# Kernel optimization log

Measured on AMD Instinct MI355X. Metric: run time of the kernel, lower is better.

Reference implementation:

```python
import jax, jax.numpy as jnp
import numpy as np

B, T, E, H = 2, 2048, 1024, 16
HS = E // H  # head size 64


def setup_inputs() -> dict:
    key = jax.random.key(0)
    ks = jax.random.split(key, 6)
    s = 0.02
    return {
        "x": jax.random.normal(ks[0], (B, T, E), dtype=jnp.float32),
        "Wq": jax.random.normal(ks[1], (E, E), dtype=jnp.float32) * s,
        "Wk": jax.random.normal(ks[2], (E, E), dtype=jnp.float32) * s,
        "Wv": jax.random.normal(ks[3], (E, E), dtype=jnp.float32) * s,
        "Wp": jax.random.normal(ks[4], (E, E), dtype=jnp.float32) * s,
        "bp": jax.random.normal(ks[5], (E,), dtype=jnp.float32) * s,
    }


def reference(x, Wq, Wk, Wv, Wp, bp):
    b, t, e = x.shape
    # per-head projections (concatenated heads == single E->E matmul, reshaped)
    def heads(w):
        return jnp.einsum('bte,ef->btf', x, w).reshape(b, t, H, HS).transpose(0, 2, 1, 3)
    q, k, v = heads(Wq), heads(Wk), heads(Wv)  # [B,H,T,HS]
    # NOTE: original scales by full embed dim E, not head_size
    scores = jnp.einsum('bhqd,bhkd->bhqk', q, k) * (e ** -0.5)
    causal = jnp.tril(jnp.ones((t, t), dtype=bool))
    scores = jnp.where(causal, scores, -jnp.inf)
    probs = jax.nn.softmax(scores, axis=-1)
    # dropout is identity in eval mode
    out = jnp.einsum('bhqk,bhkd->bhqd', probs, v)  # [B,H,T,HS]
    out = out.transpose(0, 2, 1, 3).reshape(b, t, e)
    return jnp.einsum('bte,ef->btf', out, Wp) + bp
```

## Files before the change

kernel.cpp:

```cpp
#include <hip/hip_runtime.h>
#include <math.h>

typedef __bf16 bf16x8 __attribute__((ext_vector_type(8)));
typedef __bf16 bf16x4 __attribute__((ext_vector_type(4)));
typedef float f32x4 __attribute__((ext_vector_type(4)));

constexpr int Bb = 2, Tt = 2048, Ee = 1024, Hh = 16, Hs = 64;
constexpr int Mm = Bb * Tt;

__device__ inline unsigned short f2bf(float f) {
    union { float f; unsigned u; } c; c.f = f;
    unsigned u = c.u;
    u += 0x7FFFu + ((u >> 16) & 1u);
    return (unsigned short)(u >> 16);
}

#if __has_builtin(__builtin_amdgcn_exp2f)
#define EXP2(x) __builtin_amdgcn_exp2f(x)
#else
#define EXP2(x) exp2f(x)
#endif

__device__ inline void gl2lds16(const void* g, void* l) {
    __builtin_amdgcn_global_load_lds(
        (const __attribute__((address_space(1))) void*)g,
        (__attribute__((address_space(3))) void*)l, 16, 0, 0);
}

__device__ inline unsigned pk_bf16(float a, float b) {
    union { float f; unsigned u; } ca, cb;
    ca.f = a; cb.f = b;
    return __builtin_amdgcn_perm(ca.u + 0x8000u, cb.u + 0x8000u, 0x07060302u);
}

__global__ __launch_bounds__(256) void prep(const float* __restrict__ x,
                                            const float* __restrict__ Wq,
                                            const float* __restrict__ Wk,
                                            const float* __restrict__ Wv,
                                            const float* __restrict__ Wp,
                                            unsigned short* __restrict__ xb,
                                            unsigned short* __restrict__ wt3,
                                            unsigned short* __restrict__ wpt) {
    const int tid = threadIdx.x;
    if (blockIdx.z == 4) {
        int flat = (blockIdx.y * 16 + blockIdx.x) * 256 + tid;
#pragma unroll
        for (int i = 0; i < 16; i++) {
            int gid = flat + i * 65536;
            float4 v = ((const float4*)x)[gid];
            ushort4 o;
            o.x = f2bf(v.x); o.y = f2bf(v.y); o.z = f2bf(v.z); o.w = f2bf(v.w);
            ((ushort4*)xb)[gid] = o;
        }
        return;
    }
    __shared__ unsigned short t[64][68];
    const float* W = (blockIdx.z == 0) ? Wq : (blockIdx.z == 1) ? Wk
                    : (blockIdx.z == 2) ? Wv : Wp;
    unsigned short* dst = (blockIdx.z < 3) ? wt3 + (size_t)blockIdx.z * 1024 * 1024 : wpt;
    const int k0 = blockIdx.x * 64, n0 = blockIdx.y * 64;
#pragma unroll
    for (int j = 0; j < 4; j++) {
        int row = (tid >> 4) + j * 16;
        int c4 = (tid & 15) * 4;
        float4 v = *(const float4*)&W[(size_t)(k0 + row) * 1024 + n0 + c4];
        t[row][c4 + 0] = f2bf(v.x); t[row][c4 + 1] = f2bf(v.y);
        t[row][c4 + 2] = f2bf(v.z); t[row][c4 + 3] = f2bf(v.w);
    }
    __syncthreads();
#pragma unroll
    for (int j = 0; j < 16; j++) {
        int flat = j * 256 + tid;
        int orow = flat >> 6, ocol = flat & 63;
        dst[(size_t)(n0 + orow) * 1024 + k0 + ocol] = t[ocol][orow];
    }
}

__device__ inline void gemm_mainloop(const unsigned short* __restrict__ A,
                                     const unsigned short* __restrict__ Bt,
                                     unsigned short* As, unsigned short* Bs,
                                     int bm, int bn, int tid, f32x4 (&acc)[4][4]) {
    const int lane = tid & 63, w = tid >> 6;
    const int quad = lane >> 4, cl = lane & 15;
    const int wm = (w >> 1) * 64, wn = (w & 1) * 64;

    auto stage = [&](int k0) {
#pragma unroll
        for (int i = 0; i < 2; i++) {
            int L = tid + i * 256;
            int r = L >> 2;
            int kc = (L & 3) ^ (r & 3);
            gl2lds16(A + (size_t)(bm + r) * 1024 + k0 + kc * 8, &As[L * 8]);
        }
#pragma unroll
        for (int i = 0; i < 2; i++) {
            int L = tid + i * 256;
            int r = L >> 2;
            int kc = (L & 3) ^ (r & 3);
            gl2lds16(Bt + (size_t)(bn + r) * 1024 + k0 + kc * 8, &Bs[L * 8]);
        }
    };

    stage(0);
    __syncthreads();
    for (int k0 = 0;;) {
        bf16x8 af[4], bfr[4];
#pragma unroll
        for (int mt = 0; mt < 4; mt++) {
            int r = wm + mt * 16 + cl;
            af[mt] = *(const bf16x8*)&As[(r * 4 + (quad ^ (r & 3))) * 8];
            int rb = wn + mt * 16 + cl;
            bfr[mt] = *(const bf16x8*)&Bs[(rb * 4 + (quad ^ (rb & 3))) * 8];
        }
#pragma unroll
        for (int mt = 0; mt < 4; mt++)
#pragma unroll
            for (int nt = 0; nt < 4; nt++)
                acc[mt][nt] = __builtin_amdgcn_mfma_f32_16x16x32_bf16(
                    af[mt], bfr[nt], acc[mt][nt], 0, 0, 0);
        k0 += 32;
        if (k0 >= 1024) break;
        __syncthreads();
        stage(k0);
        __syncthreads();
    }
}

__global__ __launch_bounds__(256, 2) void gemm_qkv(const unsigned short* __restrict__ A,
                                                   const unsigned short* __restrict__ Bt,
                                                   unsigned short* __restrict__ qb,
                                                   unsigned short* __restrict__ kb,
                                                   unsigned short* __restrict__ vtb) {
    __shared__ unsigned short As[128 * 32];
    __shared__ unsigned short Bs[128 * 32];
    const int tid = threadIdx.x;
    const int bm = blockIdx.y * 128;
    const int bn = blockIdx.x * 128;
    f32x4 acc[4][4] = {};
    gemm_mainloop(A, Bt, As, Bs, bm, bn, tid, acc);

    const int lane = tid & 63, w = tid >> 6;
    const int quad = lane >> 4, cl = lane & 15;
    const int wm = (w >> 1) * 64, wn = (w & 1) * 64;
    const int region = bn >> 10;

    if (region < 2) {
        unsigned short* dst = region ? kb : qb;
        const float qs = region ? 1.0f : 0.045084220027780107f;
#pragma unroll
        for (int mt = 0; mt < 4; mt++)
#pragma unroll
            for (int nt = 0; nt < 4; nt++)
#pragma unroll
                for (int rg = 0; rg < 4; rg++) {
                    int m = bm + wm + mt * 16 + quad * 4 + rg;
                    int nn = (bn + wn + nt * 16 + cl) & 1023;
                    int b = m >> 11, t = m & 2047, h = nn >> 6, hs = nn & 63;
                    dst[((size_t)(b * 16 + h) * 2048 + t) * 64 + hs] =
                        f2bf(acc[mt][nt][rg] * qs);
                }
    } else {
#pragma unroll
        for (int mt = 0; mt < 4; mt++) {
            int m0 = bm + wm + mt * 16 + quad * 4;
            int b = m0 >> 11, t0 = m0 & 2047;
#pragma unroll
            for (int nt = 0; nt < 4; nt++) {
                int nn = (bn + wn + nt * 16 + cl) & 1023;
                int h = nn >> 6, hs = nn & 63;
                ushort4 pk;
                pk.x = f2bf(acc[mt][nt][0]); pk.y = f2bf(acc[mt][nt][1]);
                pk.z = f2bf(acc[mt][nt][2]); pk.w = f2bf(acc[mt][nt][3]);
                *(ushort4*)&vtb[((size_t)(b * 16 + h) * 64 + hs) * 2048 + t0] = pk;
            }
        }
    }
}

__global__ __launch_bounds__(256, 4) void gemm_out(const unsigned short* __restrict__ A,
                                                   const unsigned short* __restrict__ Bt,
                                                   const float* __restrict__ bias,
                                                   float* __restrict__ out) {
    __shared__ unsigned short As[64 * 32];
    __shared__ unsigned short Bs[128 * 32];
    const int tid = threadIdx.x;
    const int bm = blockIdx.y * 64;
    const int bn = blockIdx.x * 128;
    const int lane = tid & 63, w = tid >> 6;
    const int quad = lane >> 4, cl = lane & 15;
    const int wm = (w >> 1) * 32, wn = (w & 1) * 64;
    f32x4 acc[2][4] = {};

    auto stage = [&](int k0) {
        {
            int L = tid;
            int r = L >> 2;
            int kc = (L & 3) ^ (r & 3);
            gl2lds16(A + (size_t)(bm + r) * 1024 + k0 + kc * 8, &As[L * 8]);
        }
#pragma unroll
        for (int i = 0; i < 2; i++) {
            int L = tid + i * 256;
            int r = L >> 2;
            int kc = (L & 3) ^ (r & 3);
            gl2lds16(Bt + (size_t)(bn + r) * 1024 + k0 + kc * 8, &Bs[L * 8]);
        }
    };

    stage(0);
    __syncthreads();
    for (int k0 = 0;;) {
        bf16x8 af[2], bfr[4];
#pragma unroll
        for (int mt = 0; mt < 2; mt++) {
            int r = wm + mt * 16 + cl;
            af[mt] = *(const bf16x8*)&As[(r * 4 + (quad ^ (r & 3))) * 8];
        }
#pragma unroll
        for (int nt = 0; nt < 4; nt++) {
            int rb = wn + nt * 16 + cl;
            bfr[nt] = *(const bf16x8*)&Bs[(rb * 4 + (quad ^ (rb & 3))) * 8];
        }
#pragma unroll
        for (int mt = 0; mt < 2; mt++)
#pragma unroll
            for (int nt = 0; nt < 4; nt++)
                acc[mt][nt] = __builtin_amdgcn_mfma_f32_16x16x32_bf16(
                    af[mt], bfr[nt], acc[mt][nt], 0, 0, 0);
        k0 += 32;
        if (k0 >= 1024) break;
        __syncthreads();
        stage(k0);
        __syncthreads();
    }

#pragma unroll
    for (int mt = 0; mt < 2; mt++)
#pragma unroll
        for (int nt = 0; nt < 4; nt++)
#pragma unroll
            for (int rg = 0; rg < 4; rg++) {
                int m = bm + wm + mt * 16 + quad * 4 + rg;
                int n = bn + wn + nt * 16 + cl;
                out[(size_t)m * 1024 + n] = acc[mt][nt][rg] + bias[n];
            }
}

__global__ __launch_bounds__(256, 2) void attn_mfma(const unsigned short* __restrict__ qg,
                                                    const unsigned short* __restrict__ kg,
                                                    const unsigned short* __restrict__ vtg,
                                                    unsigned short* __restrict__ og) {
    __shared__ unsigned short lds[36864];
    float* Cmb = (float*)lds;
    float* Ll = (float*)(lds + 8704);

    const int tid = threadIdx.x;
    const int idx = blockIdx.x;
    const int bh = idx & 31;
    const int qt = 31 - (idx >> 5);
    const int lane = tid & 63, w = tid >> 6;
    const int quad = lane >> 4, cl = lane & 15;
    const int p = w >> 1;
    const int qhalf = w & 1;
    const int qbase = qt * 64;
    const unsigned short* qB = qg + (size_t)bh * 2048 * 64;
    const unsigned short* kB = kg + (size_t)bh * 2048 * 64;
    const unsigned short* vB = vtg + (size_t)bh * 64 * 2048;

    auto stageKV = [&](int kt) {
        unsigned short* Kd = lds + (kt & 3) * 4096;
        unsigned short* Vd = lds + 16384 + (kt & 3) * 4096;
#pragma unroll
        for (int i = 0; i < 2; i++) {
            int L = tid + i * 256;
            int r = L >> 3;
            int kc = (L & 7) ^ (r & 7);
            gl2lds16(kB + (size_t)(kt * 64 + r) * 64 + kc * 8, &Kd[L * 8]);
            gl2lds16(vB + (size_t)r * 2048 + kt * 64 + kc * 8, &Vd[L * 8]);
        }
    };

    bf16x8 qf[2][2];
#pragma unroll
    for (int nt2 = 0; nt2 < 2; nt2++)
#pragma unroll
        for (int kf = 0; kf < 2; kf++) {
            int row = qbase + qhalf * 32 + nt2 * 16 + cl;
            qf[nt2][kf] = *(const bf16x8*)&qB[(size_t)row * 64 + (kf * 4 + quad) * 8];
        }

    bf16x8 ones;
#pragma unroll
    for (int i = 0; i < 8; i++) ones[i] = (__bf16)1.0f;

    f32x4 oacc[2][4] = {};
    f32x4 lacc[2] = {};
    unsigned short* Pw = lds + 32768 + w * 1024;
    const int nit = (qt + 2) >> 1;

    stageKV(0);
    if (qt >= 1) stageKV(1);
    __syncthreads();

    for (int i = 0; i < nit; i++) {
        if (2 * i + 2 <= qt) stageKV(2 * i + 2);
        if (2 * i + 3 <= qt) stageKV(2 * i + 3);

        const int kt = 2 * i + p;
        if (kt <= qt) {
            const bool diag = (kt == qt);
            const unsigned short* Kl = lds + (kt & 3) * 4096;
            const unsigned short* Vl = lds + 16384 + (kt & 3) * 4096;
            f32x4 sac[4][2] = {};
#pragma unroll
            for (int kf = 0; kf < 2; kf++)
#pragma unroll
                for (int mt = 0; mt < 4; mt++) {
                    int r = mt * 16 + cl, cc = kf * 4 + quad;
                    bf16x8 kf8 = *(const bf16x8*)&Kl[(r * 8 + (cc ^ (r & 7))) * 8];
#pragma unroll
                    for (int nt2 = 0; nt2 < 2; nt2++)
                        sac[mt][nt2] = __builtin_amdgcn_mfma_f32_16x16x32_bf16(
                            kf8, qf[nt2][kf], sac[mt][nt2], 0, 0, 0);
                }
#pragma unroll
            for (int ks = 0; ks < 2; ks++) {
#pragma unroll
                for (int mtl = 0; mtl < 2; mtl++)
#pragma unroll
                    for (int nt2 = 0; nt2 < 2; nt2++) {
                        float pv[4];
#pragma unroll
                        for (int rg = 0; rg < 4; rg++) {
                            float e = EXP2(sac[ks * 2 + mtl][nt2][rg]);
                            if (diag && (ks * 32 + mtl * 16 + quad * 4 + rg >
                                         nt2 * 16 + cl + qhalf * 32))
                                e = 0.0f;
                            pv[rg] = e;
                        }
                        uint2 d;
                        d.x = pk_bf16(pv[1], pv[0]);
                        d.y = pk_bf16(pv[3], pv[2]);
                        int r2 = nt2 * 16 + cl;
                        int c = mtl * 2 + (quad >> 1);
                        int pc = c ^ ((r2 >> 1) & 3);
                        *(uint2*)&Pw[r2 * 32 + pc * 8 + (quad & 1) * 4] = d;
                    }
                bf16x8 pf[2];
#pragma unroll
                for (int mt2 = 0; mt2 < 2; mt2++) {
                    int r2 = mt2 * 16 + cl;
                    int pc = quad ^ ((r2 >> 1) & 3);
                    pf[mt2] = *(const bf16x8*)&Pw[r2 * 32 + pc * 8];
                }
#pragma unroll
                for (int mt2 = 0; mt2 < 2; mt2++)
                    lacc[mt2] = __builtin_amdgcn_mfma_f32_16x16x32_bf16(
                        pf[mt2], ones, lacc[mt2], 0, 0, 0);
#pragma unroll
                for (int nt = 0; nt < 4; nt++) {
                    int r = nt * 16 + cl, cc = ks * 4 + quad;
                    bf16x8 vf = *(const bf16x8*)&Vl[(r * 8 + (cc ^ (r & 7))) * 8];
#pragma unroll
                    for (int mt2 = 0; mt2 < 2; mt2++)
                        oacc[mt2][nt] = __builtin_amdgcn_mfma_f32_16x16x32_bf16(
                            pf[mt2], vf, oacc[mt2][nt], 0, 0, 0);
                }
            }
        }
        __syncthreads();
    }

    if (p == 1) {
#pragma unroll
        for (int mt2 = 0; mt2 < 2; mt2++)
#pragma unroll
            for (int rg = 0; rg < 4; rg++) {
                int row = qhalf * 32 + mt2 * 16 + quad * 4 + rg;
                if (cl == 0) Ll[row] = lacc[mt2][rg];
#pragma unroll
                for (int nt = 0; nt < 4; nt++)
                    Cmb[row * 68 + nt * 16 + cl] = oacc[mt2][nt][rg];
            }
    }
    __syncthreads();
    if (p == 0) {
        const int b = bh >> 4, h = bh & 15;
#pragma unroll
        for (int mt2 = 0; mt2 < 2; mt2++)
#pragma unroll
            for (int rg = 0; rg < 4; rg++) {
                int row = qhalf * 32 + mt2 * 16 + quad * 4 + rg;
                float inv = 1.0f / (lacc[mt2][rg] + Ll[row]);
                int t = qbase + row;
#pragma unroll
                for (int nt = 0; nt < 4; nt++) {
                    int hs = nt * 16 + cl;
                    float val = oacc[mt2][nt][rg] + Cmb[row * 68 + nt * 16 + cl];
                    og[((size_t)(b * 2048 + t)) * 1024 + h * 64 + hs] = f2bf(val * inv);
                }
            }
    }
}

extern "C" void kernel_launch(void* const* d_in, const int* in_sizes, int n_in,
                              void* d_out, int out_size, void* d_ws, size_t ws_size,
                              hipStream_t stream) {
    const float* x = (const float*)d_in[0];
    const float* Wq = (const float*)d_in[1];
    const float* Wk = (const float*)d_in[2];
    const float* Wv = (const float*)d_in[3];
    const float* Wp = (const float*)d_in[4];
    const float* bp = (const float*)d_in[5];
    float* out = (float*)d_out;

    unsigned short* xb = (unsigned short*)d_ws;
    unsigned short* wt3 = xb + (size_t)Mm * Ee;
    unsigned short* wpt = wt3 + (size_t)3 * Ee * Ee;
    unsigned short* qb = wpt + (size_t)Ee * Ee;
    unsigned short* kb = qb + (size_t)Mm * Ee;
    unsigned short* vtb = kb + (size_t)Mm * Ee;
    unsigned short* ab = vtb + (size_t)Mm * Ee;

    prep<<<dim3(16, 16, 5), dim3(256), 0, stream>>>(x, Wq, Wk, Wv, Wp, xb, wt3, wpt);
    gemm_qkv<<<dim3(24, 32), dim3(256), 0, stream>>>(xb, wt3, qb, kb, vtb);
    attn_mfma<<<dim3(1024), dim3(256), 0, stream>>>(qb, kb, vtb, ab);
    gemm_out<<<dim3(8, 64), dim3(256), 0, stream>>>(ab, wpt, bp, out);
}
```

Baseline: 171.9 us.

## Rewrite QKV GEMM as 256x256 tile with double-buffered LDS pipeline

Replaces the 128x128 single-buffered QKV projection GEMM with a 256x256 tile using 512 threads, a K step of 64, and a double-buffered LDS pipeline built from hand-scheduled async global-to-LDS loads, raw s_barrier and s_waitcnt, and s_setprio around the MFMA bursts. The aim is to overlap global loads with MFMA work and get more reuse per loaded byte. In exchange it uses 128 KB of LDS per block and launches only 192 blocks. The barrier and waitcnt counts are tuned by hand, so any miscount would cause a race.

```diff
diff --git a/kernel.cpp b/kernel.cpp
--- a/kernel.cpp
+++ b/kernel.cpp
@@ -32,6 +32,10 @@
     ca.f = a; cb.f = b;
     return __builtin_amdgcn_perm(ca.u + 0x8000u, cb.u + 0x8000u, 0x07060302u);
 }
+
+#define S_BARRIER() asm volatile("s_barrier" ::: "memory")
+#define WAIT_LGKM0() asm volatile("s_waitcnt lgkmcnt(0)" ::: "memory")
+#define WAIT_VM(n) asm volatile("s_waitcnt vmcnt(" #n ")" ::: "memory")
 
 __global__ __launch_bounds__(256) void prep(const float* __restrict__ x,
                                             const float* __restrict__ Wq,
@@ -76,94 +80,152 @@
     }
 }
 
-__device__ inline void gemm_mainloop(const unsigned short* __restrict__ A,
-                                     const unsigned short* __restrict__ Bt,
-                                     unsigned short* As, unsigned short* Bs,
-                                     int bm, int bn, int tid, f32x4 (&acc)[4][4]) {
-    const int lane = tid & 63, w = tid >> 6;
-    const int quad = lane >> 4, cl = lane & 15;
-    const int wm = (w >> 1) * 64, wn = (w & 1) * 64;
-
-    auto stage = [&](int k0) {
-#pragma unroll
-        for (int i = 0; i < 2; i++) {
-            int L = tid + i * 256;
-            int r = L >> 2;
-            int kc = (L & 3) ^ (r & 3);
-            gl2lds16(A + (size_t)(bm + r) * 1024 + k0 + kc * 8, &As[L * 8]);
-        }
-#pragma unroll
-        for (int i = 0; i < 2; i++) {
-            int L = tid + i * 256;
-            int r = L >> 2;
-            int kc = (L & 3) ^ (r & 3);
-            gl2lds16(Bt + (size_t)(bn + r) * 1024 + k0 + kc * 8, &Bs[L * 8]);
-        }
-    };
-
-    stage(0);
-    __syncthreads();
-    for (int k0 = 0;;) {
-        bf16x8 af[4], bfr[4];
-#pragma unroll
-        for (int mt = 0; mt < 4; mt++) {
-            int r = wm + mt * 16 + cl;
-            af[mt] = *(const bf16x8*)&As[(r * 4 + (quad ^ (r & 3))) * 8];
-            int rb = wn + mt * 16 + cl;
-            bfr[mt] = *(const bf16x8*)&Bs[(rb * 4 + (quad ^ (rb & 3))) * 8];
-        }
-#pragma unroll
-        for (int mt = 0; mt < 4; mt++)
-#pragma unroll
-            for (int nt = 0; nt < 4; nt++)
-                acc[mt][nt] = __builtin_amdgcn_mfma_f32_16x16x32_bf16(
-                    af[mt], bfr[nt], acc[mt][nt], 0, 0, 0);
-        k0 += 32;
-        if (k0 >= 1024) break;
-        __syncthreads();
-        stage(k0);
-        __syncthreads();
-    }
-}
-
-__global__ __launch_bounds__(256, 2) void gemm_qkv(const unsigned short* __restrict__ A,
+__global__ __launch_bounds__(512, 2) void gemm_qkv(const unsigned short* __restrict__ A,
                                                    const unsigned short* __restrict__ Bt,
                                                    unsigned short* __restrict__ qb,
                                                    unsigned short* __restrict__ kb,
                                                    unsigned short* __restrict__ vtb) {
-    __shared__ unsigned short As[128 * 32];
-    __shared__ unsigned short Bs[128 * 32];
+    __shared__ unsigned short As[2][16384];
+    __shared__ unsigned short Bs[2][16384];
     const int tid = threadIdx.x;
-    const int bm = blockIdx.y * 128;
-    const int bn = blockIdx.x * 128;
-    f32x4 acc[4][4] = {};
-    gemm_mainloop(A, Bt, As, Bs, bm, bn, tid, acc);
-
+    const int bm = blockIdx.y * 256;
+    const int bn = blockIdx.x * 256;
     const int lane = tid & 63, w = tid >> 6;
     const int quad = lane >> 4, cl = lane & 15;
-    const int wm = (w >> 1) * 64, wn = (w & 1) * 64;
+    const int wm = (w >> 2) * 128;
+    const int wn = (w & 3) * 64;
+
+    f32x4 acc[8][4] = {};
+    bf16x8 a[4][2];
+    bf16x8 b[4][2];
+
+    auto stA = [&](int buf, int h, int kt) {
+#pragma unroll
+        for (int i = 0; i < 2; i++) {
+            int flat = tid + i * 512;
+            int r = flat >> 3, s = flat & 7, c = s ^ (r & 7);
+            gl2lds16(A + (size_t)(bm + h * 128 + r) * 1024 + kt * 64 + c * 8,
+                     &As[buf][h * 8192 + flat * 8]);
+        }
+    };
+    auto stB = [&](int buf, int h, int kt) {
+#pragma unroll
+        for (int i = 0; i < 2; i++) {
+            int flat = tid + i * 512;
+            int r = flat >> 3, s = flat & 7, c = s ^ (r & 7);
+            gl2lds16(Bt + (size_t)(bn + h * 128 + r) * 1024 + kt * 64 + c * 8,
+                     &Bs[buf][h * 8192 + flat * 8]);
+        }
+    };
+    auto ldA = [&](int buf, int mh) {
+#pragma unroll
+        for (int mt = 0; mt < 4; mt++) {
+            int r = wm + mh * 64 + mt * 16 + cl;
+#pragma unroll
+            for (int kf = 0; kf < 2; kf++) {
+                int c = kf * 4 + quad;
+                a[mt][kf] = *(const bf16x8*)&As[buf][r * 64 + (c ^ (r & 7)) * 8];
+            }
+        }
+    };
+    auto ldB = [&](int buf, int nh) {
+#pragma unroll
+        for (int nt = 0; nt < 2; nt++) {
+            int r = wn + nh * 32 + nt * 16 + cl;
+#pragma unroll
+            for (int kf = 0; kf < 2; kf++) {
+                int c = kf * 4 + quad;
+                b[nh * 2 + nt][kf] = *(const bf16x8*)&Bs[buf][r * 64 + (c ^ (r & 7)) * 8];
+            }
+        }
+    };
+    auto mm = [&](int mh, int nh) {
+        __builtin_amdgcn_s_setprio(1);
+#pragma unroll
+        for (int mt = 0; mt < 4; mt++)
+#pragma unroll
+            for (int nt = 0; nt < 2; nt++)
+#pragma unroll
+                for (int kf = 0; kf < 2; kf++)
+                    acc[mh * 4 + mt][nh * 2 + nt] =
+                        __builtin_amdgcn_mfma_f32_16x16x32_bf16(
+                            a[mt][kf], b[nh * 2 + nt][kf],
+                            acc[mh * 4 + mt][nh * 2 + nt], 0, 0, 0);
+        __builtin_amdgcn_s_setprio(0);
+    };
+
+    stB(0, 0, 0); stB(0, 1, 0); stA(0, 0, 0); stA(0, 1, 0);
+    stB(1, 0, 1); stB(1, 1, 1); stA(1, 0, 1);
+    WAIT_VM(6);
+    S_BARRIER();
+
+    for (int j = 0; j < 8; ++j) {
+        const int kt_b = 2 * j + 2, kt_c = 2 * j + 3;
+        const bool pf = (j < 7);
+        ldA(0, 0); ldB(0, 0);
+        stA(1, 1, 2 * j + 1);
+        S_BARRIER(); WAIT_LGKM0();
+        mm(0, 0);
+        S_BARRIER();
+        ldB(0, 1);
+        S_BARRIER(); WAIT_LGKM0();
+        mm(0, 1);
+        S_BARRIER();
+        ldA(0, 1);
+        if (pf) stB(0, 0, kt_b);
+        S_BARRIER(); WAIT_LGKM0();
+        mm(1, 1);
+        S_BARRIER();
+        if (pf) { stB(0, 1, kt_b); stA(0, 0, kt_b); }
+        if (pf) { WAIT_VM(6); } else { WAIT_VM(0); }
+        S_BARRIER();
+        mm(1, 0);
+        S_BARRIER();
+        ldA(1, 0); ldB(1, 0);
+        if (pf) stA(0, 1, kt_b);
+        S_BARRIER(); WAIT_LGKM0();
+        mm(0, 0);
+        S_BARRIER();
+        ldB(1, 1);
+        S_BARRIER(); WAIT_LGKM0();
+        mm(0, 1);
+        S_BARRIER();
+        ldA(1, 1);
+        if (pf) stB(1, 0, kt_c);
+        S_BARRIER(); WAIT_LGKM0();
+        mm(1, 1);
+        S_BARRIER();
+        if (pf) { stB(1, 1, kt_c); stA(1, 0, kt_c); }
+        WAIT_VM(6);
+        S_BARRIER();
+        mm(1, 0);
+        S_BARRIER();
+    }
+
     const int region = bn >> 10;
-
     if (region < 2) {
         unsigned short* dst = region ? kb : qb;
         const float qs = region ? 1.0f : 0.045084220027780107f;
 #pragma unroll
-        for (int mt = 0; mt < 4; mt++)
-#pragma unroll
-            for (int nt = 0; nt < 4; nt++)
+        for (int mt = 0; mt < 8; mt++)
+#pragma unroll
+            for (int nt = 0; nt < 4; nt++) {
+                int m0 = bm + wm + mt * 16 + quad * 4;
+                int nn = (bn + wn + nt * 16 + cl) & 1023;
+                int h = nn >> 6, hs = nn & 63;
 #pragma unroll
                 for (int rg = 0; rg < 4; rg++) {
-                    int m = bm + wm + mt * 16 + quad * 4 + rg;
-                    int nn = (bn + wn + nt * 16 + cl) & 1023;
-                    int b = m >> 11, t = m & 2047, h = nn >> 6, hs = nn & 63;
-                    dst[((size_t)(b * 16 + h) * 2048 + t) * 64 + hs] =
+                    int m = m0 + rg;
+                    int b2 = m >> 11, t = m & 2047;
+                    dst[((size_t)(b2 * 16 + h) * 2048 + t) * 64 + hs] =
                         f2bf(acc[mt][nt][rg] * qs);
                 }
+            }
     } else {
 #pragma unroll
-        for (int mt = 0; mt < 4; mt++) {
+        for (int mt = 0; mt < 8; mt++) {
             int m0 = bm + wm + mt * 16 + quad * 4;
-            int b = m0 >> 11, t0 = m0 & 2047;
+            int b2 = m0 >> 11, t0 = m0 & 2047;
 #pragma unroll
             for (int nt = 0; nt < 4; nt++) {
                 int nn = (bn + wn + nt * 16 + cl) & 1023;
@@ -171,7 +233,7 @@
                 ushort4 pk;
                 pk.x = f2bf(acc[mt][nt][0]); pk.y = f2bf(acc[mt][nt][1]);
                 pk.z = f2bf(acc[mt][nt][2]); pk.w = f2bf(acc[mt][nt][3]);
-                *(ushort4*)&vtb[((size_t)(b * 16 + h) * 64 + hs) * 2048 + t0] = pk;
+                *(ushort4*)&vtb[((size_t)(b2 * 16 + h) * 64 + hs) * 2048 + t0] = pk;
             }
         }
     }
@@ -423,7 +485,7 @@
     unsigned short* ab = vtb + (size_t)Mm * Ee;
 
     prep<<<dim3(16, 16, 5), dim3(256), 0, stream>>>(x, Wq, Wk, Wv, Wp, xb, wt3, wpt);
-    gemm_qkv<<<dim3(24, 32), dim3(256), 0, stream>>>(xb, wt3, qb, kb, vtb);
+    gemm_qkv<<<dim3(12, 16), dim3(512), 0, stream>>>(xb, wt3, qb, kb, vtb);
     attn_mfma<<<dim3(1024), dim3(256), 0, stream>>>(qb, kb, vtb, ab);
     gemm_out<<<dim3(8, 64), dim3(256), 0, stream>>>(ab, wpt, bp, out);
 }
```

New measurement: 177.7 us. 1.03x slower.

## Enlarge attention query tile to 128 rows with 8 waves per block

Applied to the files above, without the earlier changes.

Attention blocks now cover 128 query rows with 512 threads (8 waves) instead of 64 rows with 256 threads. Each staged K/V tile is shared by four query-row groups instead of two, which halves K/V global traffic per query. Tile scheduling changes from longest-first to an interleaved order, and causal masking now uses a per-wave offset. The cost is fewer, larger blocks (512 instead of 1024), more LDS per block, and some waves sitting idle on diagonal tiles.

```diff
diff --git a/kernel.cpp b/kernel.cpp
--- a/kernel.cpp
+++ b/kernel.cpp
@@ -246,23 +246,26 @@
             }
 }
 
-__global__ __launch_bounds__(256, 2) void attn_mfma(const unsigned short* __restrict__ qg,
+__global__ __launch_bounds__(512, 2) void attn_mfma(const unsigned short* __restrict__ qg,
                                                     const unsigned short* __restrict__ kg,
                                                     const unsigned short* __restrict__ vtg,
                                                     unsigned short* __restrict__ og) {
-    __shared__ unsigned short lds[36864];
+    __shared__ unsigned short lds[40960];
     float* Cmb = (float*)lds;
-    float* Ll = (float*)(lds + 8704);
+    float* Ll = (float*)(lds + 17408);
 
     const int tid = threadIdx.x;
     const int idx = blockIdx.x;
     const int bh = idx & 31;
-    const int qt = 31 - (idx >> 5);
+    const int hi = idx >> 5;
+    const int qt = (hi < 8) ? (15 - hi) : (hi - 8);
     const int lane = tid & 63, w = tid >> 6;
     const int quad = lane >> 4, cl = lane & 15;
-    const int p = w >> 1;
-    const int qhalf = w & 1;
-    const int qbase = qt * 64;
+    const int p = w >> 2;
+    const int qq = w & 3;
+    const int qbase = qt * 128;
+    const int row_lo = qbase + qq * 32;
+    const int kmax = 2 * qt + 1;
     const unsigned short* qB = qg + (size_t)bh * 2048 * 64;
     const unsigned short* kB = kg + (size_t)bh * 2048 * 64;
     const unsigned short* vB = vtg + (size_t)bh * 64 * 2048;
@@ -270,14 +273,11 @@
     auto stageKV = [&](int kt) {
         unsigned short* Kd = lds + (kt & 3) * 4096;
         unsigned short* Vd = lds + 16384 + (kt & 3) * 4096;
-#pragma unroll
-        for (int i = 0; i < 2; i++) {
-            int L = tid + i * 256;
-            int r = L >> 3;
-            int kc = (L & 7) ^ (r & 7);
-            gl2lds16(kB + (size_t)(kt * 64 + r) * 64 + kc * 8, &Kd[L * 8]);
-            gl2lds16(vB + (size_t)r * 2048 + kt * 64 + kc * 8, &Vd[L * 8]);
-        }
+        int L = tid;
+        int r = L >> 3;
+        int kc = (L & 7) ^ (r & 7);
+        gl2lds16(kB + (size_t)(kt * 64 + r) * 64 + kc * 8, &Kd[L * 8]);
+        gl2lds16(vB + (size_t)r * 2048 + kt * 64 + kc * 8, &Vd[L * 8]);
     };
 
     bf16x8 qf[2][2];
@@ -285,7 +285,7 @@
     for (int nt2 = 0; nt2 < 2; nt2++)
 #pragma unroll
         for (int kf = 0; kf < 2; kf++) {
-            int row = qbase + qhalf * 32 + nt2 * 16 + cl;
+            int row = row_lo + nt2 * 16 + cl;
             qf[nt2][kf] = *(const bf16x8*)&qB[(size_t)row * 64 + (kf * 4 + quad) * 8];
         }
 
@@ -296,19 +296,20 @@
     f32x4 oacc[2][4] = {};
     f32x4 lacc[2] = {};
     unsigned short* Pw = lds + 32768 + w * 1024;
-    const int nit = (qt + 2) >> 1;
+    const int nit = qt + 1;
 
     stageKV(0);
-    if (qt >= 1) stageKV(1);
+    stageKV(1);
     __syncthreads();
 
     for (int i = 0; i < nit; i++) {
-        if (2 * i + 2 <= qt) stageKV(2 * i + 2);
-        if (2 * i + 3 <= qt) stageKV(2 * i + 3);
+        if (2 * i + 2 <= kmax) stageKV(2 * i + 2);
+        if (2 * i + 3 <= kmax) stageKV(2 * i + 3);
 
         const int kt = 2 * i + p;
-        if (kt <= qt) {
-            const bool diag = (kt == qt);
+        if (kt * 64 <= row_lo + 31) {
+            const bool diag = (kt * 64 + 63 > row_lo);
+            const int d0 = row_lo - kt * 64;
             const unsigned short* Kl = lds + (kt & 3) * 4096;
             const unsigned short* Vl = lds + 16384 + (kt & 3) * 4096;
             f32x4 sac[4][2] = {};
@@ -334,7 +335,7 @@
                         for (int rg = 0; rg < 4; rg++) {
                             float e = EXP2(sac[ks * 2 + mtl][nt2][rg]);
                             if (diag && (ks * 32 + mtl * 16 + quad * 4 + rg >
-                                         nt2 * 16 + cl + qhalf * 32))
+                                         d0 + nt2 * 16 + cl))
                                 e = 0.0f;
                             pv[rg] = e;
                         }
@@ -376,7 +377,7 @@
         for (int mt2 = 0; mt2 < 2; mt2++)
 #pragma unroll
             for (int rg = 0; rg < 4; rg++) {
-                int row = qhalf * 32 + mt2 * 16 + quad * 4 + rg;
+                int row = qq * 32 + mt2 * 16 + quad * 4 + rg;
                 if (cl == 0) Ll[row] = lacc[mt2][rg];
 #pragma unroll
                 for (int nt = 0; nt < 4; nt++)
@@ -390,7 +391,7 @@
         for (int mt2 = 0; mt2 < 2; mt2++)
 #pragma unroll
             for (int rg = 0; rg < 4; rg++) {
-                int row = qhalf * 32 + mt2 * 16 + quad * 4 + rg;
+                int row = qq * 32 + mt2 * 16 + quad * 4 + rg;
                 float inv = 1.0f / (lacc[mt2][rg] + Ll[row]);
                 int t = qbase + row;
 #pragma unroll
@@ -424,6 +425,6 @@
 
     prep<<<dim3(16, 16, 5), dim3(256), 0, stream>>>(x, Wq, Wk, Wv, Wp, xb, wt3, wpt);
     gemm_qkv<<<dim3(24, 32), dim3(256), 0, stream>>>(xb, wt3, qb, kb, vtb);
-    attn_mfma<<<dim3(1024), dim3(256), 0, stream>>>(qb, kb, vtb, ab);
+    attn_mfma<<<dim3(512), dim3(512), 0, stream>>>(qb, kb, vtb, ab);
     gemm_out<<<dim3(8, 64), dim3(256), 0, stream>>>(ab, wpt, bp, out);
 }
```

New measurement: 176.8 us. 2.9% more time.

## Permute K rows at staging so P stays in registers, skipping LDS round-trip

Applied to the files above, without the earlier changes.

K rows are loaded into LDS in a permuted order, so the S=K·Q MFMA output lands in registers already laid out as the A-operand fragment for the P·V MFMA. The probabilities are packed straight into bf16x8 registers instead of being written to and read back from a per-warp LDS scratch buffer, which also shrinks shared memory. The causal mask index is updated to match the new row order. s_setprio hints are added around the MFMA sections to favour matrix issue across waves.

```diff
diff --git a/kernel.cpp b/kernel.cpp
--- a/kernel.cpp
+++ b/kernel.cpp
@@ -250,7 +250,7 @@
                                                     const unsigned short* __restrict__ kg,
                                                     const unsigned short* __restrict__ vtg,
                                                     unsigned short* __restrict__ og) {
-    __shared__ unsigned short lds[36864];
+    __shared__ unsigned short lds[32768];
     float* Cmb = (float*)lds;
     float* Ll = (float*)(lds + 8704);
 
@@ -275,7 +275,8 @@
             int L = tid + i * 256;
             int r = L >> 3;
             int kc = (L & 7) ^ (r & 7);
-            gl2lds16(kB + (size_t)(kt * 64 + r) * 64 + kc * 8, &Kd[L * 8]);
+            int grow = (r & 32) | ((r & 12) << 1) | ((r & 16) >> 2) | (r & 3);
+            gl2lds16(kB + (size_t)(kt * 64 + grow) * 64 + kc * 8, &Kd[L * 8]);
             gl2lds16(vB + (size_t)r * 2048 + kt * 64 + kc * 8, &Vd[L * 8]);
         }
     };
@@ -295,7 +296,6 @@
 
     f32x4 oacc[2][4] = {};
     f32x4 lacc[2] = {};
-    unsigned short* Pw = lds + 32768 + w * 1024;
     const int nit = (qt + 2) >> 1;
 
     stageKV(0);
@@ -312,6 +312,7 @@
             const unsigned short* Kl = lds + (kt & 3) * 4096;
             const unsigned short* Vl = lds + 16384 + (kt & 3) * 4096;
             f32x4 sac[4][2] = {};
+            __builtin_amdgcn_s_setprio(1);
 #pragma unroll
             for (int kf = 0; kf < 2; kf++)
 #pragma unroll
@@ -323,36 +324,32 @@
                         sac[mt][nt2] = __builtin_amdgcn_mfma_f32_16x16x32_bf16(
                             kf8, qf[nt2][kf], sac[mt][nt2], 0, 0, 0);
                 }
+            __builtin_amdgcn_s_setprio(0);
 #pragma unroll
             for (int ks = 0; ks < 2; ks++) {
-#pragma unroll
-                for (int mtl = 0; mtl < 2; mtl++)
-#pragma unroll
-                    for (int nt2 = 0; nt2 < 2; nt2++) {
+                bf16x8 pf[2];
+#pragma unroll
+                for (int nt2 = 0; nt2 < 2; nt2++) {
+                    unsigned dw[4];
+#pragma unroll
+                    for (int mtl = 0; mtl < 2; mtl++) {
                         float pv[4];
 #pragma unroll
                         for (int rg = 0; rg < 4; rg++) {
                             float e = EXP2(sac[ks * 2 + mtl][nt2][rg]);
-                            if (diag && (ks * 32 + mtl * 16 + quad * 4 + rg >
+                            if (diag && (ks * 32 + quad * 8 + mtl * 4 + rg >
                                          nt2 * 16 + cl + qhalf * 32))
                                 e = 0.0f;
                             pv[rg] = e;
                         }
-                        uint2 d;
-                        d.x = pk_bf16(pv[1], pv[0]);
-                        d.y = pk_bf16(pv[3], pv[2]);
-                        int r2 = nt2 * 16 + cl;
-                        int c = mtl * 2 + (quad >> 1);
-                        int pc = c ^ ((r2 >> 1) & 3);
-                        *(uint2*)&Pw[r2 * 32 + pc * 8 + (quad & 1) * 4] = d;
+                        dw[mtl * 2 + 0] = pk_bf16(pv[1], pv[0]);
+                        dw[mtl * 2 + 1] = pk_bf16(pv[3], pv[2]);
                     }
-                bf16x8 pf[2];
-#pragma unroll
-                for (int mt2 = 0; mt2 < 2; mt2++) {
-                    int r2 = mt2 * 16 + cl;
-                    int pc = quad ^ ((r2 >> 1) & 3);
-                    pf[mt2] = *(const bf16x8*)&Pw[r2 * 32 + pc * 8];
+                    union { uint4 u; bf16x8 v; } cv;
+                    cv.u = make_uint4(dw[0], dw[1], dw[2], dw[3]);
+                    pf[nt2] = cv.v;
                 }
+                __builtin_amdgcn_s_setprio(1);
 #pragma unroll
                 for (int mt2 = 0; mt2 < 2; mt2++)
                     lacc[mt2] = __builtin_amdgcn_mfma_f32_16x16x32_bf16(
@@ -366,6 +363,7 @@
                         oacc[mt2][nt] = __builtin_amdgcn_mfma_f32_16x16x32_bf16(
                             pf[mt2], vf, oacc[mt2][nt], 0, 0, 0);
                 }
+                __builtin_amdgcn_s_setprio(0);
             }
         }
         __syncthreads();
```

After: 169.0 us. About the same (-1.7%).
